# Kernel optimization log

Measured on AMD Instinct MI355X. Metric: run time of the kernel, lower is better.

The kernel has to match this reference:

```python
import jax, jax.numpy as jnp
import numpy as np

L, B, T, D, V = 2, 16, 20, 768, 30000


def setup_inputs() -> dict:
    key = jax.random.key(0)
    k1, k2, k3, k4 = jax.random.split(key, 4)
    answer_embed = jax.random.normal(k1, (L, B, T, D), dtype=jnp.float32)
    vocab_embed = 0.1 * jax.random.normal(k2, (V, D), dtype=jnp.float32)
    # classifier_transform modeled as Linear(D, D): y = x @ W.T + b
    W = jax.random.normal(k3, (D, D), dtype=jnp.float32) * (1.0 / np.sqrt(D))
    b = jax.random.normal(k4, (D,), dtype=jnp.float32) * 0.01
    return {"answer_embed": answer_embed, "vocab_embed": vocab_embed, "W": W, "b": b}


def reference(answer_embed, vocab_embed, W, b):
    # vocab_classifiers: [V, D] after the linear transform
    vocab_classifiers = vocab_embed @ W.T + b
    # Original: broadcast multiply [L,B,T,D,1]*[1,1,1,D,V] then sum over D.
    # Mathematically identical contraction over D -> [L, B, T, V]
    return jnp.einsum('lbtd,vd->lbtv', answer_embed, vocab_classifiers)
```

## Files before the change

kernel.cpp:

```cpp
#include <hip/hip_runtime.h>

#define KDIM 768
#define MANS 640
#define VV   30000
#define NGRP 235
#define NKS  (KDIM / 64)
#define VELEM (VV * KDIM)
#define CVTBLK (VELEM / 8 / 256)
#define A2BLK  ((MANS / 64) * (KDIM / 128))

typedef __attribute__((ext_vector_type(4)))  float  f32x4;
typedef __attribute__((ext_vector_type(16))) float  f32x16;
typedef __attribute__((ext_vector_type(8)))  __bf16 bf16x8;
typedef __attribute__((ext_vector_type(8)))  unsigned short ushort8;

__device__ __forceinline__ unsigned short f2bf(float f) {
    union { __bf16 h; unsigned short u; } t;
    t.h = (__bf16)f;
    return t.u;
}

__device__ __forceinline__ ushort8 cvt8(f32x4 a, f32x4 b) {
    union { bf16x8 h; ushort8 u; } c;
    c.h[0] = (__bf16)a.x; c.h[1] = (__bf16)a.y;
    c.h[2] = (__bf16)a.z; c.h[3] = (__bf16)a.w;
    c.h[4] = (__bf16)b.x; c.h[5] = (__bf16)b.y;
    c.h[6] = (__bf16)b.z; c.h[7] = (__bf16)b.w;
    return c.u;
}

__device__ __forceinline__ void load_lds16(const unsigned short* g, unsigned short* l) {
    __builtin_amdgcn_global_load_lds(
        (__attribute__((address_space(1))) void*)(void*)g,
        (__attribute__((address_space(3))) void*)l,
        16, 0, 0);
}

__device__ __forceinline__ long a2f_off(int m, int n) {
    int mb = m >> 7, wm = (m >> 6) & 1, fm = (m >> 5) & 1, colm = m & 31;
    int kt = n >> 6, g = (n >> 4) & 3, halfb = (n >> 3) & 1, e = n & 7;
    return ((((long)(mb * 12 + kt) * 2 + wm) * 2 + fm) * 4 + g) * 512
         + (halfb * 32 + colm) * 8 + e;
}


__global__ __launch_bounds__(256) void prep_small(
    const float* __restrict__ W, const float* __restrict__ A,
    const float* __restrict__ b, unsigned short* __restrict__ Wt_bf,
    float* __restrict__ cvec)
{
    __shared__ float ts[64][65];
    const int blk = blockIdx.x;
    if (blk < 144) {
        int bx = (blk % 12) * 64, by = (blk / 12) * 64;
        int tx = threadIdx.x & 63, tg = threadIdx.x >> 6;
#pragma unroll
        for (int i = 0; i < 16; ++i) {
            int r = tg * 16 + i;
            ts[r][tx] = W[(long)(by + r) * KDIM + bx + tx];
        }
        __syncthreads();
#pragma unroll
        for (int i = 0; i < 16; ++i) {
            int r = tg * 16 + i;
            Wt_bf[(long)(bx + r) * KDIM + by + tx] = f2bf(ts[tx][r]);
        }
    } else {
        int row  = (blk - 144) * 4 + (threadIdx.x >> 6);
        int lane = threadIdx.x & 63;
        const float* ap = A + (long)row * KDIM;
        float s = 0.f;
#pragma unroll
        for (int i = 0; i < KDIM / 64; ++i) s += ap[i * 64 + lane] * b[i * 64 + lane];
#pragma unroll
        for (int off = 32; off; off >>= 1) s += __shfl_down(s, off, 64);
        if (lane == 0) cvec[row] = s;
    }
}

__global__ __launch_bounds__(256) void gemm_a2(
    const float* __restrict__ Af, const unsigned short* __restrict__ Bp,
    unsigned short* __restrict__ outp,
    const float* __restrict__ vocab, unsigned short* __restrict__ vocab_vf)
{
    if (blockIdx.x >= A2BLK) {
        long id = (long)(blockIdx.x - A2BLK) * 256 + threadIdx.x;
        int  v  = (int)(id / 96);
        int  kc = (int)(id % 96);
        const float* src = vocab + (long)v * KDIM + kc * 8;
        f32x4 v0 = ((const f32x4*)src)[0], v1 = ((const f32x4*)src)[1];
        int nt = v >> 5, colv = v & 31;
        int kt = kc >> 3, g = (kc >> 1) & 3, hb = kc & 1;
        long off = ((((long)nt * 12 + kt) * 4 + g) * 64 + hb * 32 + colv) * 8;
        *(ushort8*)(vocab_vf + off) = cvt8(v0, v1);
        return;
    }

    constexpr int TM = 64, TN = 128;
    __shared__ unsigned short sA[TM * 64];
    __shared__ unsigned short sB[TN * 64];

    const int t    = threadIdx.x;
    const int lane = t & 63;
    const int w    = t >> 6;
    const int wm   = w >> 1;
    const int wn   = w & 1;
    const int half = lane >> 5;
    const int col  = lane & 31;
    const long m0  = (long)(blockIdx.x % (MANS / 64)) * TM;
    const long n0  = (long)(blockIdx.x / (MANS / 64)) * TN;

    f32x16 acc[2];
    acc[0] = (f32x16)(0.f);
    acc[1] = (f32x16)(0.f);

    const float* gaf[2]; int laOff[2];
#pragma unroll
    for (int j = 0; j < 2; ++j) {
        int s   = (j * 4 + w) * 64 + lane;
        int row = s >> 3;
        int c   = (s & 7) ^ (row & 7);
        gaf[j]   = Af + (m0 + row) * KDIM + c * 8;
        laOff[j] = s * 8;
    }
    const unsigned short* gb[4]; unsigned short* lbB[4];
#pragma unroll
    for (int j = 0; j < 4; ++j) {
        int s   = (j * 4 + w) * 64 + lane;
        int row = s >> 3;
        int c   = (s & 7) ^ (row & 7);
        gb[j]  = Bp + (n0 + row) * KDIM + c * 8;
        lbB[j] = &sB[(j * 4 + w) * 64 * 8];
    }

    for (int k0 = 0; k0 < KDIM; k0 += 64) {
#pragma unroll
        for (int j = 0; j < 4; ++j) load_lds16(gb[j] + k0, lbB[j]);
#pragma unroll
        for (int j = 0; j < 2; ++j) {
            f32x4 v0 = ((const f32x4*)(gaf[j] + k0))[0];
            f32x4 v1 = ((const f32x4*)(gaf[j] + k0))[1];
            *(ushort8*)(&sA[0] + laOff[j]) = cvt8(v0, v1);
        }
        __syncthreads();

#pragma unroll
        for (int g = 0; g < 4; ++g) {
            const int cg = g * 2 + half;
            int arow = wm * 32 + col;
            bf16x8 af = *(const bf16x8*)&sA[(arow * 8 + (cg ^ (arow & 7))) * 8];
#pragma unroll
            for (int fn = 0; fn < 2; ++fn) {
                int brow = wn * 64 + fn * 32 + col;
                bf16x8 bfv = *(const bf16x8*)&sB[(brow * 8 + (cg ^ (brow & 7))) * 8];
                acc[fn] = __builtin_amdgcn_mfma_f32_32x32x16_bf16(
                    af, bfv, acc[fn], 0, 0, 0);
            }
        }
        __syncthreads();
    }

#pragma unroll
    for (int fn = 0; fn < 2; ++fn) {
        int n = (int)n0 + wn * 64 + fn * 32 + col;
#pragma unroll
        for (int rg = 0; rg < 16; ++rg) {
            int m = (int)m0 + wm * 32 + (rg & 3) + 8 * (rg >> 2) + 4 * half;
            outp[a2f_off(m, n)] = f2bf(acc[fn][rg]);
        }
    }
}

__global__ __launch_bounds__(256) void gemm_big(
    const unsigned short* __restrict__ A, const unsigned short* __restrict__ VF,
    const float* __restrict__ cvec, float* __restrict__ outp)
{
    const int id    = blockIdx.x;
    const int x     = id & 7;
    const int q     = id >> 3;
    const int m_idx = q % 5;
    const int n_grp = (q / 5) * 8 + x;
    if (n_grp >= NGRP) return;

    const int t    = threadIdx.x;
    const int lane = t & 63;
    const int w    = t >> 6;
    const int wm   = w >> 1;
    const int wn   = w & 1;
    const int half = lane >> 5;
    const int col  = lane & 31;
    const long n0  = (long)n_grp * 128;

    f32x16 acc[2][2];
#pragma unroll
    for (int i = 0; i < 2; ++i)
#pragma unroll
        for (int j = 0; j < 2; ++j) acc[i][j] = (f32x16)(0.f);

    const unsigned short* aB = A + ((long)16 * (m_idx * 12) + 8 * wm) * 512
                                 + lane * 8;
    const unsigned short* bB = VF + (long)(n_grp * 4 + wn * 2) * 24576
                                  + lane * 8;

#pragma unroll
    for (int kt = 0; kt < NKS; ++kt) {
        const unsigned short* aK = aB + (long)kt * 8192;
        const unsigned short* bK = bB + (long)kt * 2048;
#pragma unroll
        for (int g = 0; g < 4; ++g) {
            bf16x8 af0 = *(const bf16x8*)(aK + g * 512);
            bf16x8 af1 = *(const bf16x8*)(aK + 2048 + g * 512);
            bf16x8 bf0 = *(const bf16x8*)(bK + g * 512);
            bf16x8 bf1 = *(const bf16x8*)(bK + 24576 + g * 512);
            acc[0][0] = __builtin_amdgcn_mfma_f32_32x32x16_bf16(af0, bf0, acc[0][0], 0, 0, 0);
            acc[0][1] = __builtin_amdgcn_mfma_f32_32x32x16_bf16(af0, bf1, acc[0][1], 0, 0, 0);
            acc[1][0] = __builtin_amdgcn_mfma_f32_32x32x16_bf16(af1, bf0, acc[1][0], 0, 0, 0);
            acc[1][1] = __builtin_amdgcn_mfma_f32_32x32x16_bf16(af1, bf1, acc[1][1], 0, 0, 0);
        }
    }

    const long m0 = (long)m_idx * 128;
#pragma unroll
    for (int fm = 0; fm < 2; ++fm)
#pragma unroll
        for (int fn = 0; fn < 2; ++fn) {
            long n = n0 + wn * 64 + fn * 32 + col;
            if (n < VV) {
#pragma unroll
                for (int rg = 0; rg < 16; ++rg) {
                    long m = m0 + wm * 64 + fm * 32
                           + (rg & 3) + 8 * (rg >> 2) + 4 * half;
                    outp[m * (long)VV + n] = acc[fm][fn][rg] + cvec[m];
                }
            }
        }
}

extern "C" void kernel_launch(void* const* d_in, const int* in_sizes, int n_in,
                              void* d_out, int out_size, void* d_ws, size_t ws_size,
                              hipStream_t stream) {
    const float* answer = (const float*)d_in[0];
    const float* vocab  = (const float*)d_in[1];
    const float* W      = (const float*)d_in[2];
    const float* bvec   = (const float*)d_in[3];

    char* ws = (char*)d_ws;
    unsigned short* Wt_bf   = (unsigned short*)ws;
    unsigned short* A2F     = (unsigned short*)(ws + 1179648);
    float*          cptr    = (float*)(ws + 1179648 + 983040);
    unsigned short* VF      = (unsigned short*)(ws + 2165248);

    prep_small<<<304, 256, 0, stream>>>(W, answer, bvec, Wt_bf, cptr);

    gemm_a2<<<A2BLK + CVTBLK, 256, 0, stream>>>(answer, Wt_bf, A2F, vocab, VF);

    gemm_big<<<1200, 256, 0, stream>>>(A2F, VF, cptr, (float*)d_out);
}
```

Baseline: 244.6 us.

## Double-buffer register fragments in big GEMM and retile vocab conversion per tile

The big GEMM now prefetches the next K-step's A and B fragments into a second register buffer while running MFMAs on the current one, and sets launch bounds to two blocks per SM. The vocab bf16 conversion is reorganized so each block handles one (n-tile, k-tile) pair. Out-of-range rows are clamped to the last vocab row, which pads the final partial tile and lets the GEMM clamp its tile index. The goal is to hide global-load latency behind MFMA work. The cost is higher register pressure, which the occupancy hint may turn into spills.

After: 220.5 us. 1.11x faster.

```diff
diff --git a/kernel.cpp b/kernel.cpp
--- a/kernel.cpp
+++ b/kernel.cpp
@@ -5,8 +5,8 @@
 #define VV   30000
 #define NGRP 235
 #define NKS  (KDIM / 64)
-#define VELEM (VV * KDIM)
-#define CVTBLK (VELEM / 8 / 256)
+#define NT   938
+#define CVTBLK (NT * NKS)
 #define A2BLK  ((MANS / 64) * (KDIM / 128))
 
 typedef __attribute__((ext_vector_type(4)))  float  f32x4;
@@ -84,14 +84,18 @@
     const float* __restrict__ vocab, unsigned short* __restrict__ vocab_vf)
 {
     if (blockIdx.x >= A2BLK) {
-        long id = (long)(blockIdx.x - A2BLK) * 256 + threadIdx.x;
-        int  v  = (int)(id / 96);
-        int  kc = (int)(id % 96);
-        const float* src = vocab + (long)v * KDIM + kc * 8;
+        const int bid  = blockIdx.x - A2BLK;
+        const int nt   = bid / NKS;
+        const int kt   = bid % NKS;
+        const int t    = threadIdx.x;
+        const int colv = t & 31;
+        const int hb   = (t >> 5) & 1;
+        const int g    = t >> 6;
+        long row = (long)nt * 32 + colv;
+        if (row > VV - 1) row = VV - 1;
+        const float* src = vocab + row * KDIM + kt * 64 + g * 16 + hb * 8;
         f32x4 v0 = ((const f32x4*)src)[0], v1 = ((const f32x4*)src)[1];
-        int nt = v >> 5, colv = v & 31;
-        int kt = kc >> 3, g = (kc >> 1) & 3, hb = kc & 1;
-        long off = ((((long)nt * 12 + kt) * 4 + g) * 64 + hb * 32 + colv) * 8;
+        long off = ((long)bid * 4 + g) * 512 + hb * 256 + colv * 8;
         *(ushort8*)(vocab_vf + off) = cvt8(v0, v1);
         return;
     }
@@ -171,7 +175,7 @@
     }
 }
 
-__global__ __launch_bounds__(256) void gemm_big(
+__global__ __launch_bounds__(256, 2) void gemm_big(
     const unsigned short* __restrict__ A, const unsigned short* __restrict__ VF,
     const float* __restrict__ cvec, float* __restrict__ outp)
 {
@@ -199,23 +203,47 @@
 
     const unsigned short* aB = A + ((long)16 * (m_idx * 12) + 8 * wm) * 512
                                  + lane * 8;
-    const unsigned short* bB = VF + (long)(n_grp * 4 + wn * 2) * 24576
-                                  + lane * 8;
+    int nt0 = n_grp * 4 + wn * 2;     if (nt0 > NT - 1) nt0 = NT - 1;
+    int nt1 = n_grp * 4 + wn * 2 + 1; if (nt1 > NT - 1) nt1 = NT - 1;
+    const unsigned short* bB0 = VF + (long)nt0 * 24576 + lane * 8;
+    const unsigned short* bB1 = VF + (long)nt1 * 24576 + lane * 8;
+
+    bf16x8 fa[2][2][4];
+    bf16x8 fb[2][2][4];
+
+#pragma unroll
+    for (int g = 0; g < 4; ++g) {
+        fa[0][0][g] = *(const bf16x8*)(aB + g * 512);
+        fa[0][1][g] = *(const bf16x8*)(aB + 2048 + g * 512);
+        fb[0][0][g] = *(const bf16x8*)(bB0 + g * 512);
+        fb[0][1][g] = *(const bf16x8*)(bB1 + g * 512);
+    }
 
 #pragma unroll
     for (int kt = 0; kt < NKS; ++kt) {
-        const unsigned short* aK = aB + (long)kt * 8192;
-        const unsigned short* bK = bB + (long)kt * 2048;
+        const int cur = kt & 1, nxt = cur ^ 1;
+        if (kt < NKS - 1) {
+            const unsigned short* aK = aB + (long)(kt + 1) * 8192;
+            const unsigned short* bK0 = bB0 + (long)(kt + 1) * 2048;
+            const unsigned short* bK1 = bB1 + (long)(kt + 1) * 2048;
+#pragma unroll
+            for (int g = 0; g < 4; ++g) {
+                fa[nxt][0][g] = *(const bf16x8*)(aK + g * 512);
+                fa[nxt][1][g] = *(const bf16x8*)(aK + 2048 + g * 512);
+                fb[nxt][0][g] = *(const bf16x8*)(bK0 + g * 512);
+                fb[nxt][1][g] = *(const bf16x8*)(bK1 + g * 512);
+            }
+        }
 #pragma unroll
         for (int g = 0; g < 4; ++g) {
-            bf16x8 af0 = *(const bf16x8*)(aK + g * 512);
-            bf16x8 af1 = *(const bf16x8*)(aK + 2048 + g * 512);
-            bf16x8 bf0 = *(const bf16x8*)(bK + g * 512);
-            bf16x8 bf1 = *(const bf16x8*)(bK + 24576 + g * 512);
-            acc[0][0] = __builtin_amdgcn_mfma_f32_32x32x16_bf16(af0, bf0, acc[0][0], 0, 0, 0);
-            acc[0][1] = __builtin_amdgcn_mfma_f32_32x32x16_bf16(af0, bf1, acc[0][1], 0, 0, 0);
-            acc[1][0] = __builtin_amdgcn_mfma_f32_32x32x16_bf16(af1, bf0, acc[1][0], 0, 0, 0);
-            acc[1][1] = __builtin_amdgcn_mfma_f32_32x32x16_bf16(af1, bf1, acc[1][1], 0, 0, 0);
+            acc[0][0] = __builtin_amdgcn_mfma_f32_32x32x16_bf16(
+                fa[cur][0][g], fb[cur][0][g], acc[0][0], 0, 0, 0);
+            acc[0][1] = __builtin_amdgcn_mfma_f32_32x32x16_bf16(
+                fa[cur][0][g], fb[cur][1][g], acc[0][1], 0, 0, 0);
+            acc[1][0] = __builtin_amdgcn_mfma_f32_32x32x16_bf16(
+                fa[cur][1][g], fb[cur][0][g], acc[1][0], 0, 0, 0);
+            acc[1][1] = __builtin_amdgcn_mfma_f32_32x32x16_bf16(
+                fa[cur][1][g], fb[cur][1][g], acc[1][1], 0, 0, 0);
         }
     }
 
```
